# Kernel optimization log

Hardware: AMD Instinct MI355X
Metric: run time of the kernel (lower is better)

## Reference

```python
import jax, jax.numpy as jnp
import numpy as np

B, C, H, W = 2, 256, 64, 64
HEADS, DIM_HEAD = 8, 64
INNER = HEADS * DIM_HEAD


def setup_inputs() -> dict:
    key = jax.random.key(0)
    k1, k2, k3, k4 = jax.random.split(key, 4)
    x = jax.random.normal(k1, (B, C, H, W), dtype=jnp.float32)
    # 1x1 conv weights stored as [out_ch, in_ch]
    w_qkv = jax.random.normal(k2, (3 * INNER, C), dtype=jnp.float32) * (1.0 / np.sqrt(C))
    w_out = jax.random.normal(k3, (C, INNER), dtype=jnp.float32) * (1.0 / np.sqrt(INNER))
    b_out = jax.random.normal(k4, (C,), dtype=jnp.float32) * 0.01
    return {"x": x, "w_qkv": w_qkv, "w_out": w_out, "b_out": b_out}


def reference(x, w_qkv, w_out, b_out):
    b, c, h, w = x.shape
    n = h * w
    # 1x1 conv == channel matmul
    qkv = jnp.einsum('oc,bchw->bohw', w_qkv, x)  # [B, 3*inner, H, W]
    qkv = qkv.reshape(b, 3, HEADS, DIM_HEAD, n)
    qkv = jnp.transpose(qkv, (1, 0, 2, 4, 3))    # [3, B, heads, N, dim_head]
    q, k, v = qkv[0], qkv[1], qkv[2]
    scale = 1.0 / (DIM_HEAD ** 0.5)
    dots = jnp.einsum('bhnd,bhmd->bhnm', q, k) * scale  # [B, heads, N, N]
    attn = jax.nn.softmax(dots, axis=-1)
    out = jnp.einsum('bhnm,bhmd->bhnd', attn, v)        # [B, heads, N, dim_head]
    out = jnp.transpose(out, (0, 1, 3, 2)).reshape(b, INNER, h, w)
    return jnp.einsum('ci,bihw->bchw', w_out, out) + b_out[None, :, None, None]
```

## Files before the change

### kernel.cpp

```cpp
#include <hip/hip_runtime.h>
#include <hip/hip_bf16.h>

typedef unsigned short u16;
typedef __attribute__((ext_vector_type(8))) short bf16x8;
typedef __attribute__((ext_vector_type(4))) float f32x4;
typedef __attribute__((ext_vector_type(8))) unsigned short u16x8;
typedef __attribute__((ext_vector_type(4))) unsigned short u16x4;

#define N_POS 4096
#define HEADS 8
#define DHEAD 64
#define CIN   256
#define INNER 512
#define NSPLIT 2
#define JCHUNK (N_POS / NSPLIT)

__device__ __forceinline__ u16 f2bf(float f) {
    union { float f; unsigned int u; } v; v.f = f;
    unsigned int u = v.u + 0x7FFFu + ((v.u >> 16) & 1u);
    return (u16)(u >> 16);
}

__device__ __forceinline__ unsigned int pkbf2(float lo, float hi) {
    union { __hip_bfloat162 b; unsigned int u; } cv;
    cv.b = __float22bfloat162_rn(make_float2(lo, hi));
    return cv.u;
}

__global__ __launch_bounds__(256) void k0_prep(const float* __restrict__ x,
                                               const float* __restrict__ w_qkv,
                                               const float* __restrict__ w_out,
                                               u16* __restrict__ xT,
                                               u16* __restrict__ wq,
                                               u16* __restrict__ wo) {
    int bid = blockIdx.x;
    int t   = threadIdx.x;
    if (bid < 256) {
        int b = bid >> 7, rest = bid & 127;
        int n  = (rest & 15) * 256 + t;
        int c0 = (rest >> 4) * 32;
        const float* xp = x + (size_t)b * CIN * N_POS + n;
        u16* op = xT + ((size_t)(b * N_POS + n)) * CIN + c0;
        for (int g = 0; g < 4; ++g) {
            u16x8 v;
            for (int j = 0; j < 8; ++j)
                v[j] = f2bf(xp[(size_t)(c0 + g * 8 + j) * N_POS]);
            *(u16x8*)(op + g * 8) = v;
        }
    } else if (bid < 448) {
        size_t idx = (size_t)(bid - 256) * 2048 + t * 8;
        u16x8 v;
        for (int j = 0; j < 8; ++j) v[j] = f2bf(w_qkv[idx + j]);
        *(u16x8*)(wq + idx) = v;
    } else {
        size_t idx = (size_t)(bid - 448) * 2048 + t * 8;
        u16x8 v;
        for (int j = 0; j < 8; ++j) v[j] = f2bf(w_out[idx + j]);
        *(u16x8*)(wo + idx) = v;
    }
}

__global__ __launch_bounds__(256, 4) void k1_qkv(const u16* __restrict__ wq,
                                                 const u16* __restrict__ xT,
                                                 u16* __restrict__ q_ws,
                                                 u16* __restrict__ k_ws,
                                                 u16* __restrict__ vt_ws) {
    __shared__ u16 Alds[64 * 40];
    __shared__ u16 Blds[128 * 40];
    int tid = threadIdx.x;
    int n0  = blockIdx.x * 128;
    int by  = blockIdx.y;
    int b   = blockIdx.z;
    int o0  = by * 64;
    int sel = by >> 3;
    int h   = by & 7;
    int wv = tid >> 6, l = tid & 63, quad = l >> 4, l15 = l & 15;
    int srow = tid >> 2, sseg = tid & 3;
    int brow = tid >> 1, bseg = tid & 1;

    f32x4 acc[8] = {};
    for (int c0 = 0; c0 < CIN; c0 += 32) {
        *(u16x8*)&Alds[srow * 40 + sseg * 8] =
            *(const u16x8*)(wq + (size_t)(o0 + srow) * CIN + c0 + sseg * 8);
        const u16* xp = xT + ((size_t)(b * N_POS + n0 + brow)) * CIN + c0 + bseg * 16;
        *(u16x8*)&Blds[brow * 40 + bseg * 16]     = *(const u16x8*)xp;
        *(u16x8*)&Blds[brow * 40 + bseg * 16 + 8] = *(const u16x8*)(xp + 8);
        __syncthreads();
        bf16x8 af = *(const bf16x8*)&Alds[(wv * 16 + l15) * 40 + quad * 8];
        for (int nt = 0; nt < 8; ++nt) {
            bf16x8 bfrag = *(const bf16x8*)&Blds[(nt * 16 + l15) * 40 + quad * 8];
            acc[nt] = __builtin_amdgcn_mfma_f32_16x16x32_bf16(af, bfrag, acc[nt], 0, 0, 0);
        }
        __syncthreads();
    }
    const float QSCALE = 0.125f * 1.44269504088896f;
    float sc = (sel == 0) ? QSCALE : 1.0f;
    int dbase = wv * 16 + quad * 4;
    for (int nt = 0; nt < 8; ++nt) {
        int n = n0 + nt * 16 + l15;
        if (sel < 2) {
            u16* base = (sel == 0) ? q_ws : k_ws;
            u16x4 pk;
            for (int r = 0; r < 4; ++r) pk[r] = f2bf(acc[nt][r] * sc);
            *(u16x4*)&base[((size_t)((b * HEADS + h) * N_POS + n)) * DHEAD + dbase] = pk;
        } else {
            for (int r = 0; r < 4; ++r)
                vt_ws[((size_t)((b * HEADS + h) * DHEAD + dbase + r)) * N_POS + n] =
                    f2bf(acc[nt][r]);
        }
    }
}

__global__ __launch_bounds__(256, 2) void k2_attn(const u16* __restrict__ q_ws,
                                                  const u16* __restrict__ k_ws,
                                                  const u16* __restrict__ vt_ws,
                                                  float* __restrict__ op_ws,
                                                  float* __restrict__ lw_ws) {
    __shared__ u16 Klds[64 * 72];
    __shared__ u16 Vlds[64 * 72];
    int tid = threadIdx.x;
    int q0  = blockIdx.x * 256;
    int bh  = blockIdx.y;
    int half = blockIdx.z;
    int jbase = half * JCHUNK;
    int wv = tid >> 6, l = tid & 63, quad = l >> 4, l15 = l & 15;
    int srow = tid >> 2, sseg = tid & 3;
    int srowp = (srow & 0x23) | ((srow & 4) << 2) | ((srow & 0x18) >> 1);

    const u16* qp = q_ws + ((size_t)(bh * N_POS + q0 + wv * 64 + l15)) * DHEAD + quad * 8;
    bf16x8 bq[4][2];
    for (int it = 0; it < 4; ++it) {
        bq[it][0] = *(const bf16x8*)(qp + (size_t)it * 16 * DHEAD);
        bq[it][1] = *(const bf16x8*)(qp + (size_t)it * 16 * DHEAD + 32);
    }

    f32x4 Oacc[4][4] = {};
    float lsum[4] = {0.f, 0.f, 0.f, 0.f};

    const u16* kp = k_ws + ((size_t)(bh * N_POS + srow)) * DHEAD + sseg * 16;
    const u16* vp = vt_ws + ((size_t)(bh * DHEAD + srow)) * N_POS + sseg * 16;

    u16x8 pf0 = *(const u16x8*)(kp + (size_t)jbase * DHEAD);
    u16x8 pf1 = *(const u16x8*)(kp + (size_t)jbase * DHEAD + 8);
    u16x8 pf2 = *(const u16x8*)(vp + jbase);
    u16x8 pf3 = *(const u16x8*)(vp + jbase + 8);

    for (int j0 = jbase; j0 < jbase + JCHUNK; j0 += 64) {
        *(u16x8*)&Klds[srowp * 72 + sseg * 16]     = pf0;
        *(u16x8*)&Klds[srowp * 72 + sseg * 16 + 8] = pf1;
        *(u16x8*)&Vlds[srow * 72 + sseg * 16]      = pf2;
        *(u16x8*)&Vlds[srow * 72 + sseg * 16 + 8]  = pf3;
        __syncthreads();

        if (j0 + 64 < jbase + JCHUNK) {
            const u16* kpj = kp + (size_t)(j0 + 64) * DHEAD;
            pf0 = *(const u16x8*)kpj;
            pf1 = *(const u16x8*)(kpj + 8);
            pf2 = *(const u16x8*)(vp + j0 + 64);
            pf3 = *(const u16x8*)(vp + j0 + 72);
        }

        unsigned int pkw[4][2][4];
        for (int p = 0; p < 2; ++p)
            for (int a = 0; a < 2; ++a) {
                const u16* kb = &Klds[((2 * p + a) * 16 + l15) * 72 + quad * 8];
                bf16x8 kf0 = *(const bf16x8*)kb;
                bf16x8 kf1 = *(const bf16x8*)(kb + 32);
                f32x4 z[4];
                for (int it = 0; it < 4; ++it) {
                    f32x4 t = {};
                    t = __builtin_amdgcn_mfma_f32_16x16x32_bf16(kf0, bq[it][0], t, 0, 0, 0);
                    t = __builtin_amdgcn_mfma_f32_16x16x32_bf16(kf1, bq[it][1], t, 0, 0, 0);
                    z[it] = t;
                }
                for (int it = 0; it < 4; ++it) {
                    float e0 = __builtin_amdgcn_exp2f(z[it][0]);
                    float e1 = __builtin_amdgcn_exp2f(z[it][1]);
                    float e2 = __builtin_amdgcn_exp2f(z[it][2]);
                    float e3 = __builtin_amdgcn_exp2f(z[it][3]);
                    lsum[it] += (e0 + e1) + (e2 + e3);
                    pkw[it][p][2 * a]     = pkbf2(e0, e1);
                    pkw[it][p][2 * a + 1] = pkbf2(e2, e3);
                }
            }

        for (int dt = 0; dt < 4; ++dt)
            for (int p = 0; p < 2; ++p) {
                bf16x8 vf = *(const bf16x8*)&Vlds[(dt * 16 + l15) * 72 + p * 32 + quad * 8];
                for (int it = 0; it < 4; ++it) {
                    union { unsigned int u[4]; bf16x8 v; } cv;
                    cv.u[0] = pkw[it][p][0]; cv.u[1] = pkw[it][p][1];
                    cv.u[2] = pkw[it][p][2]; cv.u[3] = pkw[it][p][3];
                    Oacc[it][dt] = __builtin_amdgcn_mfma_f32_16x16x32_bf16(vf, cv.v, Oacc[it][dt], 0, 0, 0);
                }
            }
        __syncthreads();
    }

    int b = bh >> 3, h = bh & 7;
    float* opb = op_ws + (size_t)half * 2 * N_POS * INNER;
    float* lwb = lw_ws + (size_t)half * 2 * HEADS * N_POS;
    for (int it = 0; it < 4; ++it) {
        float ls = lsum[it];
        ls += __shfl_xor(ls, 16);
        ls += __shfl_xor(ls, 32);
        int n = q0 + wv * 64 + it * 16 + l15;
        if (quad == 0) lwb[(size_t)bh * N_POS + n] = ls;
        float* dst = opb + ((size_t)(b * N_POS + n)) * INNER + h * DHEAD;
        for (int dt = 0; dt < 4; ++dt)
            *(f32x4*)&dst[dt * 16 + quad * 4] = Oacc[it][dt];
    }
}

__global__ __launch_bounds__(256) void k3_out(const u16* __restrict__ wo,
                                              const float* __restrict__ b_out,
                                              const float* __restrict__ op_ws,
                                              const float* __restrict__ lw_ws,
                                              float* __restrict__ out) {
    __shared__ u16 Alds[64 * 40];
    __shared__ u16 Blds[64 * 40];
    int tid = threadIdx.x;
    int n0 = blockIdx.x * 64;
    int c0 = blockIdx.y * 64;
    int b  = blockIdx.z;
    int wv = tid >> 6, l = tid & 63, quad = l >> 4, l15 = l & 15;
    int srow = tid >> 2, sseg = tid & 3;

    f32x4 acc[4] = {};
    for (int i0 = 0; i0 < INNER; i0 += 32) {
        *(u16x8*)&Alds[srow * 40 + sseg * 8] =
            *(const u16x8*)(wo + (size_t)(c0 + srow) * INNER + i0 + sseg * 8);
        {
            int i = i0 + sseg * 8;
            int h = i >> 6;
            int n = n0 + srow;
            size_t lidx = ((size_t)(b * HEADS + h)) * N_POS + n;
            float ls = lw_ws[lidx] + lw_ws[(size_t)2 * HEADS * N_POS + lidx];
            float inv = 1.0f / ls;
            const float* p0 = op_ws + ((size_t)(b * N_POS + n)) * INNER + i;
            const float* p1 = p0 + (size_t)2 * N_POS * INNER;
            f32x4 a0 = *(const f32x4*)p0, a1 = *(const f32x4*)(p0 + 4);
            f32x4 b0 = *(const f32x4*)p1, b1 = *(const f32x4*)(p1 + 4);
            u16x8 v;
            for (int k = 0; k < 4; ++k) v[k]     = f2bf((a0[k] + b0[k]) * inv);
            for (int k = 0; k < 4; ++k) v[4 + k] = f2bf((a1[k] + b1[k]) * inv);
            *(u16x8*)&Blds[srow * 40 + sseg * 8] = v;
        }
        __syncthreads();
        bf16x8 af = *(const bf16x8*)&Alds[(wv * 16 + l15) * 40 + quad * 8];
        for (int nt = 0; nt < 4; ++nt) {
            bf16x8 bfrag = *(const bf16x8*)&Blds[(nt * 16 + l15) * 40 + quad * 8];
            acc[nt] = __builtin_amdgcn_mfma_f32_16x16x32_bf16(af, bfrag, acc[nt], 0, 0, 0);
        }
        __syncthreads();
    }
    for (int r = 0; r < 4; ++r) {
        int c = c0 + wv * 16 + quad * 4 + r;
        float bias = b_out[c];
        for (int nt = 0; nt < 4; ++nt) {
            int n = n0 + nt * 16 + l15;
            out[((size_t)(b * CIN + c)) * N_POS + n] = acc[nt][r] + bias;
        }
    }
}

extern "C" void kernel_launch(void* const* d_in, const int* in_sizes, int n_in,
                              void* d_out, int out_size, void* d_ws, size_t ws_size,
                              hipStream_t stream) {
    const float* x     = (const float*)d_in[0];
    const float* w_qkv = (const float*)d_in[1];
    const float* w_out = (const float*)d_in[2];
    const float* b_out = (const float*)d_in[3];
    float* out = (float*)d_out;

    u16* ws    = (u16*)d_ws;
    u16* xT    = ws;
    u16* q_ws  = xT   + (size_t)2 * N_POS * CIN;
    u16* k_ws  = q_ws + (size_t)2 * HEADS * N_POS * DHEAD;
    u16* vt_ws = k_ws + (size_t)2 * HEADS * N_POS * DHEAD;
    u16* wq_bf = vt_ws + (size_t)2 * HEADS * N_POS * DHEAD;
    u16* wo_bf = wq_bf + (size_t)3 * INNER * CIN;
    float* op_ws = (float*)(wo_bf + (size_t)CIN * INNER);
    float* lw_ws = op_ws + (size_t)NSPLIT * 2 * N_POS * INNER;

    hipLaunchKernelGGL(k0_prep, dim3(512), dim3(256), 0, stream,
                       x, w_qkv, w_out, xT, wq_bf, wo_bf);
    hipLaunchKernelGGL(k1_qkv, dim3(32, 24, 2), dim3(256), 0, stream,
                       wq_bf, xT, q_ws, k_ws, vt_ws);
    hipLaunchKernelGGL(k2_attn, dim3(16, 16, NSPLIT), dim3(256), 0, stream,
                       q_ws, k_ws, vt_ws, op_ws, lw_ws);
    hipLaunchKernelGGL(k3_out, dim3(64, 4, 2), dim3(256), 0, stream,
                       wo_bf, b_out, op_ws, lw_ws, out);
}
```

Measured before the change: 178.7 us.

## Split attention keys four ways and store partial outputs in bf16

Raises the key-dimension split from 2 to 4, so the attention grid doubles to 1024 blocks, and raises the occupancy hint in launch_bounds to 4 blocks per CU. The per-split partial outputs are written as bf16 instead of fp32, which keeps workspace traffic roughly unchanged despite twice as many partials. The output kernel now sums four partials and four softmax denominators. The aim is better CU utilisation in the attention stage. The cost is extra reduction work, bf16 rounding of partial sums, and register pressure from the tighter launch bound.

```diff
diff --git a/kernel.cpp b/kernel.cpp
--- a/kernel.cpp
+++ b/kernel.cpp
@@ -12,13 +12,19 @@
 #define DHEAD 64
 #define CIN   256
 #define INNER 512
-#define NSPLIT 2
+#define NSPLIT 4
 #define JCHUNK (N_POS / NSPLIT)
 
 __device__ __forceinline__ u16 f2bf(float f) {
     union { float f; unsigned int u; } v; v.f = f;
     unsigned int u = v.u + 0x7FFFu + ((v.u >> 16) & 1u);
     return (u16)(u >> 16);
+}
+
+__device__ __forceinline__ float b2f(u16 x) {
+    union { float f; unsigned int u; } v;
+    v.u = ((unsigned int)x) << 16;
+    return v.f;
 }
 
 __device__ __forceinline__ unsigned int pkbf2(float lo, float hi) {
@@ -111,10 +117,10 @@
     }
 }
 
-__global__ __launch_bounds__(256, 2) void k2_attn(const u16* __restrict__ q_ws,
+__global__ __launch_bounds__(256, 4) void k2_attn(const u16* __restrict__ q_ws,
                                                   const u16* __restrict__ k_ws,
                                                   const u16* __restrict__ vt_ws,
-                                                  float* __restrict__ op_ws,
+                                                  u16* __restrict__ op_ws,
                                                   float* __restrict__ lw_ws) {
     __shared__ u16 Klds[64 * 72];
     __shared__ u16 Vlds[64 * 72];
@@ -198,7 +204,7 @@
     }
 
     int b = bh >> 3, h = bh & 7;
-    float* opb = op_ws + (size_t)half * 2 * N_POS * INNER;
+    u16* opb   = op_ws + (size_t)half * 2 * N_POS * INNER;
     float* lwb = lw_ws + (size_t)half * 2 * HEADS * N_POS;
     for (int it = 0; it < 4; ++it) {
         float ls = lsum[it];
@@ -206,15 +212,18 @@
         ls += __shfl_xor(ls, 32);
         int n = q0 + wv * 64 + it * 16 + l15;
         if (quad == 0) lwb[(size_t)bh * N_POS + n] = ls;
-        float* dst = opb + ((size_t)(b * N_POS + n)) * INNER + h * DHEAD;
-        for (int dt = 0; dt < 4; ++dt)
-            *(f32x4*)&dst[dt * 16 + quad * 4] = Oacc[it][dt];
+        u16* dst = opb + ((size_t)(b * N_POS + n)) * INNER + h * DHEAD;
+        for (int dt = 0; dt < 4; ++dt) {
+            u16x4 w;
+            for (int r = 0; r < 4; ++r) w[r] = f2bf(Oacc[it][dt][r]);
+            *(u16x4*)&dst[dt * 16 + quad * 4] = w;
+        }
     }
 }
 
 __global__ __launch_bounds__(256) void k3_out(const u16* __restrict__ wo,
                                               const float* __restrict__ b_out,
-                                              const float* __restrict__ op_ws,
+                                              const u16* __restrict__ op_ws,
                                               const float* __restrict__ lw_ws,
                                               float* __restrict__ out) {
     __shared__ u16 Alds[64 * 40];
@@ -235,16 +244,19 @@
             int h = i >> 6;
             int n = n0 + srow;
             size_t lidx = ((size_t)(b * HEADS + h)) * N_POS + n;
-            float ls = lw_ws[lidx] + lw_ws[(size_t)2 * HEADS * N_POS + lidx];
+            float ls = 0.f;
+            for (int s = 0; s < NSPLIT; ++s)
+                ls += lw_ws[(size_t)s * 2 * HEADS * N_POS + lidx];
             float inv = 1.0f / ls;
-            const float* p0 = op_ws + ((size_t)(b * N_POS + n)) * INNER + i;
-            const float* p1 = p0 + (size_t)2 * N_POS * INNER;
-            f32x4 a0 = *(const f32x4*)p0, a1 = *(const f32x4*)(p0 + 4);
-            f32x4 b0 = *(const f32x4*)p1, b1 = *(const f32x4*)(p1 + 4);
-            u16x8 v;
-            for (int k = 0; k < 4; ++k) v[k]     = f2bf((a0[k] + b0[k]) * inv);
-            for (int k = 0; k < 4; ++k) v[4 + k] = f2bf((a1[k] + b1[k]) * inv);
-            *(u16x8*)&Blds[srow * 40 + sseg * 8] = v;
+            const u16* p = op_ws + ((size_t)(b * N_POS + n)) * INNER + i;
+            float a8[8] = {};
+            for (int s = 0; s < NSPLIT; ++s) {
+                u16x8 v = *(const u16x8*)(p + (size_t)s * 2 * N_POS * INNER);
+                for (int k = 0; k < 8; ++k) a8[k] += b2f(v[k]);
+            }
+            u16x8 o;
+            for (int k = 0; k < 8; ++k) o[k] = f2bf(a8[k] * inv);
+            *(u16x8*)&Blds[srow * 40 + sseg * 8] = o;
         }
         __syncthreads();
         bf16x8 af = *(const bf16x8*)&Alds[(wv * 16 + l15) * 40 + quad * 8];
@@ -280,8 +292,8 @@
     u16* vt_ws = k_ws + (size_t)2 * HEADS * N_POS * DHEAD;
     u16* wq_bf = vt_ws + (size_t)2 * HEADS * N_POS * DHEAD;
     u16* wo_bf = wq_bf + (size_t)3 * INNER * CIN;
-    float* op_ws = (float*)(wo_bf + (size_t)CIN * INNER);
-    float* lw_ws = op_ws + (size_t)NSPLIT * 2 * N_POS * INNER;
+    u16* op_ws = wo_bf + (size_t)CIN * INNER;
+    float* lw_ws = (float*)(op_ws + (size_t)NSPLIT * 2 * N_POS * INNER);
 
     hipLaunchKernelGGL(k0_prep, dim3(512), dim3(256), 0, stream,
                        x, w_qkv, w_out, xT, wq_bf, wo_bf);
```

New measurement: 534.4 us. 199% more time.
